# Kernel tuning notes

Measured on AMD Instinct MI355X. Metric: run time of the kernel, lower is better.

Reference implementation:

```python
import jax, jax.numpy as jnp
import numpy as np
from jax.ops import segment_sum

N_NODES = 50000


def graph_conv(src, dst, x, W, b, n_nodes):
    # DGL GraphConv with norm='both' (allow_zero_in_degree=True):
    # h = D_in^{-1/2} * A^T (D_out^{-1/2} * x) W + b, degrees clamped to >=1
    ones = jnp.ones(src.shape[0], dtype=x.dtype)
    deg_out = jnp.clip(segment_sum(ones, src, num_segments=n_nodes), 1.0)
    deg_in = jnp.clip(segment_sum(ones, dst, num_segments=n_nodes), 1.0)
    h = x * jax.lax.rsqrt(deg_out)[:, None]
    h = h @ W                      # apply weight before aggregation (mult_W first)
    m = segment_sum(h[src], dst, num_segments=n_nodes)  # sparse neighbor sum
    return m * jax.lax.rsqrt(deg_in)[:, None] + b


def setup_inputs() -> dict:
    key = jax.random.key(0)
    ks = jax.random.split(key, 10)
    n, e = N_NODES, 1600000
    d_in, h1, h2, h3 = 128, 128, 128, 64
    in_feat = jax.random.normal(ks[0], (n, d_in), dtype=jnp.float32)
    src = jax.random.randint(ks[1], (e,), 0, n, dtype=jnp.int32)
    dst = jax.random.randint(ks[2], (e,), 0, n, dtype=jnp.int32)
    s = lambda fi, fo: (1.0 / np.sqrt(fi)).astype(np.float32)
    W1 = jax.random.normal(ks[3], (d_in, h1), dtype=jnp.float32) * s(d_in, h1)
    b1 = jnp.zeros((h1,), dtype=jnp.float32)
    W2 = jax.random.normal(ks[4], (h1, h2), dtype=jnp.float32) * s(h1, h2)
    b2 = jnp.zeros((h2,), dtype=jnp.float32)
    Wf = jax.random.normal(ks[5], (h2, h3), dtype=jnp.float32) * s(h2, h3)
    bf = jnp.zeros((h3,), dtype=jnp.float32)
    return {"in_feat": in_feat, "src": src, "dst": dst,
            "W1": W1, "b1": b1, "W2": W2, "b2": b2, "Wf": Wf, "bf": bf}


def reference(in_feat, src, dst, W1, b1, W2, b2, Wf, bf):
    n = in_feat.shape[0]
    h = graph_conv(src, dst, in_feat, W1, b1, n)
    h = jax.nn.relu(h)
    # dropout(p=0.2) is identity in eval mode
    h = graph_conv(src, dst, h, W2, b2, n)
    return h @ Wf + bf
```

## Files before the change

kernel.cpp:

```cpp
#include <hip/hip_runtime.h>
#include <hip/hip_fp16.h>

#define FD 128
#define OD 64
#define RN 256
#define CHUNKS 256
#define NRMAX 1024

typedef _Float16 f16x8 __attribute__((ext_vector_type(8)));
typedef float    f32x4 __attribute__((ext_vector_type(4)));
typedef float    f32x2 __attribute__((ext_vector_type(2)));


__global__ __launch_bounds__(1024) void region_hist_kernel(const int* __restrict__ src,
                                                           const int* __restrict__ dst,
                                                           int* __restrict__ hist_g,
                                                           int* __restrict__ hist_gs,
                                                           int E, int NR, int CS) {
    __shared__ int hist[NRMAX];
    __shared__ int hist_s[NRMAX];
    int c = blockIdx.x;
    for (int t = threadIdx.x; t < NR; t += 1024) { hist[t] = 0; hist_s[t] = 0; }
    __syncthreads();
    int e0 = c * CS, e1 = min(e0 + CS, E);
    int nv = (e1 - e0) & ~3;
    for (int e = e0 + threadIdx.x * 4; e < e0 + nv; e += 4096) {
        int4 d = *(const int4*)(dst + e);
        int4 s = *(const int4*)(src + e);
        atomicAdd(&hist[d.x >> 8], 1);
        atomicAdd(&hist[d.y >> 8], 1);
        atomicAdd(&hist[d.z >> 8], 1);
        atomicAdd(&hist[d.w >> 8], 1);
        atomicAdd(&hist_s[s.x >> 8], 1);
        atomicAdd(&hist_s[s.y >> 8], 1);
        atomicAdd(&hist_s[s.z >> 8], 1);
        atomicAdd(&hist_s[s.w >> 8], 1);
    }
    for (int e = e0 + nv + threadIdx.x; e < e1; e += 1024) {
        atomicAdd(&hist[dst[e] >> 8], 1);
        atomicAdd(&hist_s[src[e] >> 8], 1);
    }
    __syncthreads();
    for (int t = threadIdx.x; t < NR; t += 1024) {
        hist_g[t * CHUNKS + c]  = hist[t];
        hist_gs[t * CHUNKS + c] = hist_s[t];
    }
}

__global__ __launch_bounds__(1024) void scanfold_kernel(const int* __restrict__ hist_g,
                                                        const int* __restrict__ hist_gs,
                                                        int* __restrict__ rstart,
                                                        int* __restrict__ cursor,
                                                        int* __restrict__ sstart,
                                                        int* __restrict__ scursor,
                                                        int NR, int E,
                                                        const float* __restrict__ W2,
                                                        const float* __restrict__ Wf,
                                                        const float* __restrict__ b2,
                                                        const float* __restrict__ bf,
                                                        const float* __restrict__ W1,
                                                        __half* __restrict__ W1t,
                                                        __half* __restrict__ Wct,
                                                        float* __restrict__ bc) {
    __shared__ int wsum[16];
    int tid = threadIdx.x, lane = tid & 63, w = tid >> 6;

    if (blockIdx.x >= 1) {
        int gid = (blockIdx.x - 1) * 1024 + tid;
        if (gid < FD * FD) {
            int col = gid >> 7, k = gid & 127;
            W1t[gid] = __float2half(W1[k * FD + col]);
        }
        if (gid < FD * OD) {
            int col = gid >> 7, k = gid & 127;
            float s = 0.f;
            for (int kk = 0; kk < FD; kk++) s += W2[k * FD + kk] * Wf[kk * OD + col];
            Wct[gid] = __float2half(s);
        }
        if (gid < OD) {
            float s = bf[gid];
            for (int k = 0; k < FD; k++) s += b2[k] * Wf[k * OD + gid];
            bc[gid] = s;
        }
        return;
    }

    int total = 0;
    if (tid < NR) {
        const int4* hp = (const int4*)(hist_g + (size_t)tid * CHUNKS);
        #pragma unroll 8
        for (int c4 = 0; c4 < CHUNKS / 4; c4++) {
            int4 h = hp[c4];
            total += h.x + h.y + h.z + h.w;
        }
    }
    int x = total;
    #pragma unroll
    for (int d = 1; d < 64; d <<= 1) {
        int t = __shfl_up(x, d, 64);
        if (lane >= d) x += t;
    }
    if (lane == 63) wsum[w] = x;
    __syncthreads();
    if (w == 0) {
        int s = (lane < 16) ? wsum[lane] : 0;
        #pragma unroll
        for (int d = 1; d < 16; d <<= 1) {
            int t = __shfl_up(s, d, 64);
            if (lane >= d) s += t;
        }
        if (lane < 16) wsum[lane] = s;
    }
    __syncthreads();
    int off = (w == 0) ? 0 : wsum[w - 1];
    if (tid < NR) {
        int start = x + off - total;
        rstart[tid] = start;
        int run = start;
        const int4* hp = (const int4*)(hist_g + (size_t)tid * CHUNKS);
        int4* cp = (int4*)(cursor + (size_t)tid * CHUNKS);
        #pragma unroll 8
        for (int c4 = 0; c4 < CHUNKS / 4; c4++) {
            int4 h = hp[c4];
            int4 o;
            o.x = run; run += h.x;
            o.y = run; run += h.y;
            o.z = run; run += h.z;
            o.w = run; run += h.w;
            cp[c4] = o;
        }
    }
    if (tid == 0) rstart[NR] = E;
    __syncthreads();
    total = 0;
    if (tid < NR) {
        const int4* hp = (const int4*)(hist_gs + (size_t)tid * CHUNKS);
        #pragma unroll 8
        for (int c4 = 0; c4 < CHUNKS / 4; c4++) {
            int4 h = hp[c4];
            total += h.x + h.y + h.z + h.w;
        }
    }
    x = total;
    #pragma unroll
    for (int d = 1; d < 64; d <<= 1) {
        int t = __shfl_up(x, d, 64);
        if (lane >= d) x += t;
    }
    if (lane == 63) wsum[w] = x;
    __syncthreads();
    if (w == 0) {
        int s = (lane < 16) ? wsum[lane] : 0;
        #pragma unroll
        for (int d = 1; d < 16; d <<= 1) {
            int t = __shfl_up(s, d, 64);
            if (lane >= d) s += t;
        }
        if (lane < 16) wsum[lane] = s;
    }
    __syncthreads();
    off = (w == 0) ? 0 : wsum[w - 1];
    if (tid < NR) {
        int start = x + off - total;
        sstart[tid] = start;
        int run = start;
        const int4* hp = (const int4*)(hist_gs + (size_t)tid * CHUNKS);
        int4* cp = (int4*)(scursor + (size_t)tid * CHUNKS);
        #pragma unroll 8
        for (int c4 = 0; c4 < CHUNKS / 4; c4++) {
            int4 h = hp[c4];
            int4 o;
            o.x = run; run += h.x;
            o.y = run; run += h.y;
            o.z = run; run += h.z;
            o.w = run; run += h.w;
            cp[c4] = o;
        }
    }
    if (tid == 0) sstart[NR] = E;
}

__global__ __launch_bounds__(1024) void partition_kernel(const int* __restrict__ src,
                                                         const int* __restrict__ dst,
                                                         const int* __restrict__ cursor,
                                                         const int* __restrict__ scursor,
                                                         int* __restrict__ epack,
                                                         unsigned char* __restrict__ spack,
                                                         int E, int NR, int CS) {
    __shared__ int cur[NRMAX];
    __shared__ int scur[NRMAX];
    int c = blockIdx.x;
    for (int t = threadIdx.x; t < NR; t += 1024) {
        cur[t]  = cursor[(size_t)t * CHUNKS + c];
        scur[t] = scursor[(size_t)t * CHUNKS + c];
    }
    __syncthreads();
    int e0 = c * CS, e1 = min(e0 + CS, E);
    int nv = (e1 - e0) & ~3;
    for (int e = e0 + threadIdx.x * 4; e < e0 + nv; e += 4096) {
        int4 d = *(const int4*)(dst + e);
        int4 s = *(const int4*)(src + e);
        int p0 = atomicAdd(&cur[d.x >> 8], 1);
        int p1 = atomicAdd(&cur[d.y >> 8], 1);
        int p2 = atomicAdd(&cur[d.z >> 8], 1);
        int p3 = atomicAdd(&cur[d.w >> 8], 1);
        epack[p0] = ((d.x & 255) << 17) | s.x;
        epack[p1] = ((d.y & 255) << 17) | s.y;
        epack[p2] = ((d.z & 255) << 17) | s.z;
        epack[p3] = ((d.w & 255) << 17) | s.w;
        int q0 = atomicAdd(&scur[s.x >> 8], 1);
        int q1 = atomicAdd(&scur[s.y >> 8], 1);
        int q2 = atomicAdd(&scur[s.z >> 8], 1);
        int q3 = atomicAdd(&scur[s.w >> 8], 1);
        spack[q0] = (unsigned char)(s.x & 255);
        spack[q1] = (unsigned char)(s.y & 255);
        spack[q2] = (unsigned char)(s.z & 255);
        spack[q3] = (unsigned char)(s.w & 255);
    }
    for (int e = e0 + nv + threadIdx.x; e < e1; e += 1024) {
        int d = dst[e], s = src[e];
        int pos = atomicAdd(&cur[d >> 8], 1);
        epack[pos] = ((d & 255) << 17) | s;
        int qos = atomicAdd(&scur[s >> 8], 1);
        spack[qos] = (unsigned char)(s & 255);
    }
}

__global__ __launch_bounds__(1024) void region_finish_kernel(const int* __restrict__ epack,
                                                             const int* __restrict__ rstart,
                                                             const unsigned char* __restrict__ spack,
                                                             const int* __restrict__ sstart,
                                                             const float* __restrict__ in_feat,
                                                             int* __restrict__ csrc,
                                                             int* __restrict__ row_start,
                                                             float* __restrict__ r_in,
                                                             float* __restrict__ r_out,
                                                             __half* __restrict__ Xs,
                                                             int N, int NR, int E) {
    __shared__ int cnt[RN];
    __shared__ int cur[RN];
    __shared__ int wsum[16];
    __shared__ float rloc[RN];
    const int r = blockIdx.x, tid = threadIdx.x;
    const int lane = tid & 63, w = tid >> 6;

    const int s0 = rstart[r], s1 = rstart[r + 1];
    if (tid < RN) cnt[tid] = 0;
    __syncthreads();
    for (int e = s0 + tid; e < s1; e += 1024)
        atomicAdd(&cnt[epack[e] >> 17], 1);
    __syncthreads();
    int cv = (tid < RN) ? cnt[tid] : 0;
    int x = cv;
    #pragma unroll
    for (int d = 1; d < 64; d <<= 1) {
        int t = __shfl_up(x, d, 64);
        if (lane >= d) x += t;
    }
    if (lane == 63 && w < 4) wsum[w] = x;
    __syncthreads();
    if (tid < RN) {
        int woff = 0;
        for (int i = 0; i < w; i++) woff += wsum[i];
        int start = s0 + x - cv + woff;
        cur[tid] = start;
        int node = r * RN + tid;
        if (node < N) {
            row_start[node] = start;
            r_in[node] = rsqrtf((float)max(cv, 1));
        }
    }
    if (r == NR - 1 && tid == 0) row_start[N] = E;
    __syncthreads();
    for (int e = s0 + tid; e < s1; e += 1024) {
        int pk = epack[e];
        int pos = atomicAdd(&cur[pk >> 17], 1);
        csrc[pos] = pk & 0x1FFFF;
    }
    __syncthreads();

    const int t0 = sstart[r], t1 = sstart[r + 1];
    if (tid < RN) cnt[tid] = 0;
    __syncthreads();
    for (int e = t0 + tid; e < t1; e += 1024)
        atomicAdd(&cnt[spack[e]], 1);
    __syncthreads();
    if (tid < RN) {
        float ro = rsqrtf((float)max(cnt[tid], 1));
        rloc[tid] = ro;
        int node = r * RN + tid;
        if (node < N) r_out[node] = ro;
    }
    __syncthreads();

    for (int idx = tid; idx < RN * 32; idx += 1024) {
        int nrow = idx >> 5;
        int node = r * RN + nrow;
        if (node >= N) break;
        int gi = node * 32 + (idx & 31);
        float ro = rloc[nrow];
        float4 t = ((const float4*)in_feat)[gi];
        ((__half2*)Xs)[2 * gi]     = __floats2half2_rn(t.x * ro, t.y * ro);
        ((__half2*)Xs)[2 * gi + 1] = __floats2half2_rn(t.z * ro, t.w * ro);
    }
}

__global__ __launch_bounds__(1024, 8) void fused1_kernel(const __half* __restrict__ Xs,
                                                         const float* __restrict__ r_in,
                                                         const float* __restrict__ r_out,
                                                         const int* __restrict__ rs,
                                                         const int* __restrict__ csrc,
                                                         const __half* __restrict__ W1t,
                                                         const float* __restrict__ b1,
                                                         const __half* __restrict__ Wct,
                                                         __half* __restrict__ tbuf,
                                                         int N) {
    const int tid = threadIdx.x;
    const int lane = tid & 63, w = tid >> 6;
    const int l15 = lane & 15, quad = lane >> 4;
    const int base = blockIdx.x * 16;
    __shared__ __half2  zt[16][68];
    __shared__ _Float16 yt[16][136];

    {
        const int v = base + w;
        float ax = 0.f, ay = 0.f;
        if (v < N) {
            int s0 = __builtin_amdgcn_readfirstlane(rs[v]);
            int s1 = __builtin_amdgcn_readfirstlane(rs[v + 1]);
            const int deg = s1 - s0;
            const int nb = deg >> 4;
            int e = s0;
            if (nb) {
                int ia[16];
                #pragma unroll
                for (int u = 0; u < 16; u++) ia[u] = csrc[e + u];
                for (int b = 1; b < nb; b++) {
                    __half2 t[16];
                    #pragma unroll
                    for (int u = 0; u < 16; u++)
                        t[u] = ((const __half2*)(Xs + (size_t)ia[u] * FD))[lane];
                    int eb = e + (b << 4);
                    #pragma unroll
                    for (int u = 0; u < 16; u++) ia[u] = csrc[eb + u];
                    #pragma unroll
                    for (int u = 0; u < 16; u++) {
                        float2 f = __half22float2(t[u]);
                        ax += f.x; ay += f.y;
                    }
                }
                __half2 t[16];
                #pragma unroll
                for (int u = 0; u < 16; u++)
                    t[u] = ((const __half2*)(Xs + (size_t)ia[u] * FD))[lane];
                #pragma unroll
                for (int u = 0; u < 16; u++) {
                    float2 f = __half22float2(t[u]);
                    ax += f.x; ay += f.y;
                }
                e += nb << 4;
            }
            const int rem = s1 - e;
            if (rem) {
                const int last = s1 - 1;
                int ia[16];
                #pragma unroll
                for (int u = 0; u < 16; u++) ia[u] = csrc[min(e + u, last)];
                #pragma unroll
                for (int u = 0; u < 16; u++) {
                    unsigned raw = ((const unsigned*)(Xs + (size_t)ia[u] * FD))[lane];
                    raw = (u < rem) ? raw : 0u;
                    union { unsigned q; __half2 h; } tt; tt.q = raw;
                    float2 f = __half22float2(tt.h);
                    ax += f.x; ay += f.y;
                }
            }
            float ri = r_in[v];
            zt[w][lane] = __floats2half2_rn(ax * ri, ay * ri);
        } else {
            zt[w][lane] = __floats2half2_rn(0.f, 0.f);
        }
    }
    __syncthreads();

    if (w < 8) {
        const int col = 16 * w + l15;
        const f16x8* bp = (const f16x8*)((const _Float16*)W1t + (size_t)col * FD + quad * 8);
        f16x8 bf[4];
        #pragma unroll
        for (int kk = 0; kk < 4; kk++) bf[kk] = bp[kk * 4];
        const _Float16* Arow = (const _Float16*)&zt[l15][0] + quad * 8;
        f16x8 afrag[4];
        #pragma unroll
        for (int kk = 0; kk < 4; kk++) afrag[kk] = *(const f16x8*)(Arow + kk * 32);
        f32x4 acc = {0.f, 0.f, 0.f, 0.f};
        #pragma unroll
        for (int kk = 0; kk < 4; kk++)
            acc = __builtin_amdgcn_mfma_f32_16x16x32_f16(afrag[kk], bf[kk], acc, 0, 0, 0);
        float bb = b1[col];
        #pragma unroll
        for (int r = 0; r < 4; r++) {
            int row = quad * 4 + r;
            int v = base + row;
            float rsc = (v < N) ? r_out[v] : 0.f;
            yt[row][col] = (_Float16)(fmaxf(acc[r] + bb, 0.f) * rsc);
        }
    }
    __syncthreads();

    if (w < 4) {
        const int col = 16 * w + l15;
        const f16x8* bp = (const f16x8*)((const _Float16*)Wct + (size_t)col * FD + quad * 8);
        f16x8 bf[4];
        #pragma unroll
        for (int kk = 0; kk < 4; kk++) bf[kk] = bp[kk * 4];
        const _Float16* Arow = &yt[l15][0] + quad * 8;
        f16x8 afrag[4];
        #pragma unroll
        for (int kk = 0; kk < 4; kk++) afrag[kk] = *(const f16x8*)(Arow + kk * 32);
        f32x4 acc = {0.f, 0.f, 0.f, 0.f};
        #pragma unroll
        for (int kk = 0; kk < 4; kk++)
            acc = __builtin_amdgcn_mfma_f32_16x16x32_f16(afrag[kk], bf[kk], acc, 0, 0, 0);
        #pragma unroll
        for (int r = 0; r < 4; r++) {
            int row = quad * 4 + r;
            int v = base + row;
            if (v < N)
                tbuf[(size_t)v * OD + col] = __float2half(acc[r]);
        }
    }
}

__global__ __launch_bounds__(256) void agg64_kernel(const __half* __restrict__ T,
                                                    const float* __restrict__ r_in,
                                                    const int* __restrict__ rs,
                                                    const int* __restrict__ csrc,
                                                    const float* __restrict__ bc,
                                                    float* __restrict__ out, int N) {
    const int tid = threadIdx.x;
    const int lane = tid & 63, wv = tid >> 6;
    const int hf = lane >> 5, l32 = lane & 31;
    int v = blockIdx.x * 8 + wv * 2 + hf;
    if (v >= N) return;
    int s0 = rs[v], s1 = rs[v + 1];
    const int deg = s1 - s0;
    float ax = 0.f, ay = 0.f;
    const int nb = deg >> 3;
    int e = s0;
    if (nb) {
        int ia[8];
        #pragma unroll
        for (int u = 0; u < 8; u++) ia[u] = csrc[e + u];
        for (int b = 1; b < nb; b++) {
            __half2 t[8];
            #pragma unroll
            for (int u = 0; u < 8; u++)
                t[u] = ((const __half2*)(T + (size_t)ia[u] * OD))[l32];
            int eb = e + (b << 3);
            #pragma unroll
            for (int u = 0; u < 8; u++) ia[u] = csrc[eb + u];
            #pragma unroll
            for (int u = 0; u < 8; u++) {
                float2 f = __half22float2(t[u]);
                ax += f.x; ay += f.y;
            }
        }
        __half2 t[8];
        #pragma unroll
        for (int u = 0; u < 8; u++)
            t[u] = ((const __half2*)(T + (size_t)ia[u] * OD))[l32];
        #pragma unroll
        for (int u = 0; u < 8; u++) {
            float2 f = __half22float2(t[u]);
            ax += f.x; ay += f.y;
        }
        e += nb << 3;
    }
    const int rem = s1 - e;
    if (rem) {
        const int last = s1 - 1;
        int ia[8];
        #pragma unroll
        for (int u = 0; u < 8; u++) ia[u] = csrc[min(e + u, last)];
        #pragma unroll
        for (int u = 0; u < 8; u++) {
            unsigned raw = ((const unsigned*)(T + (size_t)ia[u] * OD))[l32];
            raw = (u < rem) ? raw : 0u;
            union { unsigned q; __half2 h; } tt; tt.q = raw;
            float2 f = __half22float2(tt.h);
            ax += f.x; ay += f.y;
        }
    }
    float ri = r_in[v];
    f32x2 o;
    o.x = ax * ri + bc[l32 * 2];
    o.y = ay * ri + bc[l32 * 2 + 1];
    __builtin_nontemporal_store(o, (f32x2*)(out + (size_t)v * OD) + l32);
}

extern "C" void kernel_launch(void* const* d_in, const int* in_sizes, int n_in,
                              void* d_out, int out_size, void* d_ws, size_t ws_size,
                              hipStream_t stream) {
    const float* in_feat = (const float*)d_in[0];
    const int*   src     = (const int*)d_in[1];
    const int*   dst     = (const int*)d_in[2];
    const float* W1      = (const float*)d_in[3];
    const float* b1      = (const float*)d_in[4];
    const float* W2      = (const float*)d_in[5];
    const float* b2      = (const float*)d_in[6];
    const float* Wf      = (const float*)d_in[7];
    const float* bf      = (const float*)d_in[8];
    float* out = (float*)d_out;

    const int N = in_sizes[0] / FD;
    const int E = in_sizes[1];
    const int NR = (N + RN - 1) / RN;
    const int CS = (((E + CHUNKS - 1) / CHUNKS) + 3) & ~3;

    char* ws = (char*)d_ws;
    size_t off = 0;
    auto alloc = [&](size_t bytes) -> void* {
        void* p = ws + off;
        off += (bytes + 255) / 256 * 256;
        return p;
    };
    unsigned char* spack = (unsigned char*)alloc((size_t)E);
    int*    epack   = (int*)alloc((size_t)E * 4);
    __half* tbuf    = (__half*)spack;
    float*  r_out   = (float*)alloc((size_t)N * 4);
    float*  r_in    = (float*)alloc((size_t)N * 4);
    int*    hist_g  = (int*)alloc((size_t)CHUNKS * NRMAX * 4);
    int*    hist_gs = (int*)alloc((size_t)CHUNKS * NRMAX * 4);
    int*    cursor  = (int*)alloc((size_t)CHUNKS * NRMAX * 4);
    int*    scursor = (int*)alloc((size_t)CHUNKS * NRMAX * 4);
    int*    rstart  = (int*)alloc((size_t)(NR + 1) * 4);
    int*    sstart  = (int*)alloc((size_t)(NR + 1) * 4);
    int*    csrc    = (int*)alloc((size_t)E * 4);
    int*    row_start = (int*)alloc((size_t)(N + 1) * 4);
    __half* Xs      = (__half*)alloc((size_t)N * FD * 2);
    __half* W1t     = (__half*)alloc((size_t)FD * FD * 2);
    __half* Wct     = (__half*)alloc((size_t)OD * FD * 2);
    float*  bc      = (float*)alloc((size_t)OD * 4);
    (void)ws_size; (void)n_in; (void)out_size;

    region_hist_kernel<<<CHUNKS, 1024, 0, stream>>>(src, dst, hist_g, hist_gs, E, NR, CS);
    scanfold_kernel<<<17, 1024, 0, stream>>>(hist_g, hist_gs, rstart, cursor, sstart, scursor,
                                             NR, E, W2, Wf, b2, bf, W1, W1t, Wct, bc);
    partition_kernel<<<CHUNKS, 1024, 0, stream>>>(src, dst, cursor, scursor, epack, spack, E, NR, CS);
    region_finish_kernel<<<NR, 1024, 0, stream>>>(epack, rstart, spack, sstart, in_feat,
                                                  csrc, row_start, r_in, r_out, Xs, N, NR, E);
    fused1_kernel<<<(N + 15) / 16, 1024, 0, stream>>>(Xs, r_in, r_out, row_start, csrc,
                                                      W1t, b1, Wct, tbuf, N);
    agg64_kernel<<<(N + 7) / 8, 256, 0, stream>>>(tbuf, r_in, row_start, csrc, bc, out, N);
}
```

Baseline: 257.5 us.

## Process 64 nodes per block with dynamic wave work queue in fused1

The fused aggregation+GEMM kernel now handles 64 nodes per 1024-thread block instead of 16. Waves pull node indices from a shared atomic counter, which balances uneven degrees inside the block. W1 fragments are loaded once per wave and reused over two row tiles, and all 16 waves take part in both MFMA stages instead of 8 and 4. The cost is more LDS per block, which lowers occupancy, plus a shared atomic and a shuffle per node.

```diff
diff --git a/kernel.cpp b/kernel.cpp
--- a/kernel.cpp
+++ b/kernel.cpp
@@ -6,6 +6,7 @@
 #define RN 256
 #define CHUNKS 256
 #define NRMAX 1024
+#define BN 64
 
 typedef _Float16 f16x8 __attribute__((ext_vector_type(8)));
 typedef float    f32x4 __attribute__((ext_vector_type(4)));
@@ -318,12 +319,26 @@
     const int tid = threadIdx.x;
     const int lane = tid & 63, w = tid >> 6;
     const int l15 = lane & 15, quad = lane >> 4;
-    const int base = blockIdx.x * 16;
-    __shared__ __half2  zt[16][68];
-    __shared__ _Float16 yt[16][136];
-
+    const int base = blockIdx.x * BN;
+    __shared__ __half2  zt[BN][68];
+    __shared__ _Float16 yt[BN][136];
+    __shared__ int nctr;
+
+    if (tid == 0) nctr = 16;
+
+    const int ct1 = w & 7;
+    const int colB1 = ct1 * 16 + l15;
+    f16x8 bf1[4];
     {
-        const int v = base + w;
+        const f16x8* bp = (const f16x8*)((const _Float16*)W1t + (size_t)colB1 * FD + quad * 8);
+        #pragma unroll
+        for (int kk = 0; kk < 4; kk++) bf1[kk] = bp[kk * 4];
+    }
+    __syncthreads();
+
+    int n = w;
+    while (n < BN) {
+        const int v = base + n;
         float ax = 0.f, ay = 0.f;
         if (v < N) {
             int s0 = __builtin_amdgcn_readfirstlane(rs[v]);
@@ -376,58 +391,62 @@
                 }
             }
             float ri = r_in[v];
-            zt[w][lane] = __floats2half2_rn(ax * ri, ay * ri);
+            zt[n][lane] = __floats2half2_rn(ax * ri, ay * ri);
         } else {
-            zt[w][lane] = __floats2half2_rn(0.f, 0.f);
-        }
-    }
-    __syncthreads();
-
-    if (w < 8) {
-        const int col = 16 * w + l15;
-        const f16x8* bp = (const f16x8*)((const _Float16*)W1t + (size_t)col * FD + quad * 8);
-        f16x8 bf[4];
-        #pragma unroll
-        for (int kk = 0; kk < 4; kk++) bf[kk] = bp[kk * 4];
-        const _Float16* Arow = (const _Float16*)&zt[l15][0] + quad * 8;
+            zt[n][lane] = __floats2half2_rn(0.f, 0.f);
+        }
+        int nn;
+        if (lane == 0) nn = atomicAdd(&nctr, 1);
+        n = __shfl(nn, 0);
+    }
+    __syncthreads();
+
+    #pragma unroll
+    for (int t2 = 0; t2 < 2; t2++) {
+        const int t = w + 16 * t2;
+        const int rt = t >> 3;
+        const int r0 = rt * 16;
+        const _Float16* Arow = (const _Float16*)&zt[r0 + l15][0] + quad * 8;
         f16x8 afrag[4];
         #pragma unroll
         for (int kk = 0; kk < 4; kk++) afrag[kk] = *(const f16x8*)(Arow + kk * 32);
         f32x4 acc = {0.f, 0.f, 0.f, 0.f};
         #pragma unroll
         for (int kk = 0; kk < 4; kk++)
-            acc = __builtin_amdgcn_mfma_f32_16x16x32_f16(afrag[kk], bf[kk], acc, 0, 0, 0);
-        float bb = b1[col];
+            acc = __builtin_amdgcn_mfma_f32_16x16x32_f16(afrag[kk], bf1[kk], acc, 0, 0, 0);
+        float bb = b1[colB1];
         #pragma unroll
         for (int r = 0; r < 4; r++) {
-            int row = quad * 4 + r;
+            int row = r0 + quad * 4 + r;
             int v = base + row;
             float rsc = (v < N) ? r_out[v] : 0.f;
-            yt[row][col] = (_Float16)(fmaxf(acc[r] + bb, 0.f) * rsc);
-        }
-    }
-    __syncthreads();
-
-    if (w < 4) {
-        const int col = 16 * w + l15;
-        const f16x8* bp = (const f16x8*)((const _Float16*)Wct + (size_t)col * FD + quad * 8);
-        f16x8 bf[4];
-        #pragma unroll
-        for (int kk = 0; kk < 4; kk++) bf[kk] = bp[kk * 4];
-        const _Float16* Arow = &yt[l15][0] + quad * 8;
+            yt[row][colB1] = (_Float16)(fmaxf(acc[r] + bb, 0.f) * rsc);
+        }
+    }
+    __syncthreads();
+
+    {
+        const int rt = w >> 2, ct = w & 3;
+        const int colB2 = ct * 16 + l15;
+        const f16x8* bp = (const f16x8*)((const _Float16*)Wct + (size_t)colB2 * FD + quad * 8);
+        f16x8 bf2[4];
+        #pragma unroll
+        for (int kk = 0; kk < 4; kk++) bf2[kk] = bp[kk * 4];
+        const int r0 = rt * 16;
+        const _Float16* Arow = &yt[r0 + l15][0] + quad * 8;
         f16x8 afrag[4];
         #pragma unroll
         for (int kk = 0; kk < 4; kk++) afrag[kk] = *(const f16x8*)(Arow + kk * 32);
         f32x4 acc = {0.f, 0.f, 0.f, 0.f};
         #pragma unroll
         for (int kk = 0; kk < 4; kk++)
-            acc = __builtin_amdgcn_mfma_f32_16x16x32_f16(afrag[kk], bf[kk], acc, 0, 0, 0);
+            acc = __builtin_amdgcn_mfma_f32_16x16x32_f16(afrag[kk], bf2[kk], acc, 0, 0, 0);
         #pragma unroll
         for (int r = 0; r < 4; r++) {
-            int row = quad * 4 + r;
+            int row = r0 + quad * 4 + r;
             int v = base + row;
             if (v < N)
-                tbuf[(size_t)v * OD + col] = __float2half(acc[r]);
+                tbuf[(size_t)v * OD + colB2] = __float2half(acc[r]);
         }
     }
 }
@@ -550,7 +569,7 @@
     partition_kernel<<<CHUNKS, 1024, 0, stream>>>(src, dst, cursor, scursor, epack, spack, E, NR, CS);
     region_finish_kernel<<<NR, 1024, 0, stream>>>(epack, rstart, spack, sstart, in_feat,
                                                   csrc, row_start, r_in, r_out, Xs, N, NR, E);
-    fused1_kernel<<<(N + 15) / 16, 1024, 0, stream>>>(Xs, r_in, r_out, row_start, csrc,
-                                                      W1t, b1, Wct, tbuf, N);
+    fused1_kernel<<<(N + BN - 1) / BN, 1024, 0, stream>>>(Xs, r_in, r_out, row_start, csrc,
+                                                          W1t, b1, Wct, tbuf, N);
     agg64_kernel<<<(N + 7) / 8, 256, 0, stream>>>(tbuf, r_in, row_start, csrc, bc, out, N);
 }
```

Result: no change. 256.7 us (-0.3%).
